# Optimization experiments

Measured on AMD Instinct MI355X. Metric: run time of the kernel, lower is better.

Reference implementation:

```python
import jax, jax.numpy as jnp
import numpy as np

B, C, L = 16, 256, 2048

def setup_inputs() -> dict:
    key = jax.random.key(0)
    k1, k2, k3, k4 = jax.random.split(key, 4)
    return {
        "proj_query": jax.random.normal(k1, (B, C, L), dtype=jnp.float32),
        "proj_key": jax.random.normal(k2, (B, C, L), dtype=jnp.float32),
        "proj_val": jax.random.normal(k3, (B, C, L), dtype=jnp.float32),
        "padding_mask": jax.random.uniform(k4, (B, 1, L), dtype=jnp.float32),
    }

def reference(proj_query, proj_key, proj_val, padding_mask):
    c = proj_query.shape[1]
    # energy[b,l,m] = sum_c Q[b,c,l] * K[b,c,m]  -> (B, L, L)
    energy = jnp.einsum("bcl,bcm->blm", proj_query, proj_key) / jnp.sqrt(jnp.float32(c))
    # log-additive padding mask (the tril mask in the source is dead code, never applied)
    logits = energy + jnp.log(padding_mask + 1e-9)
    attention = jax.nn.softmax(logits, axis=-1)
    # post-softmax multiplicative mask
    attention = attention * padding_mask
    # out[b,c,l] = sum_m V[b,c,m] * attention[b,l,m]  -> (B, C, L)
    out = jnp.einsum("bcm,blm->bcl", proj_val, attention)
    return out
```

## Files before the change

kernel.cpp:

```cpp
#include <hip/hip_runtime.h>
#include <hip/hip_bf16.h>

#define B_ 16
#define C_ 256
#define L_ 2048
#define MT 32

typedef __attribute__((ext_vector_type(8))) short bf16x8;
typedef __attribute__((ext_vector_type(4))) float f32x4;

__device__ __forceinline__ short f2bf_rne(float f) {
    union { float f; unsigned u; } x; x.f = f;
    unsigned r = x.u + 0x7fffu + ((x.u >> 16) & 1u);
    return (short)(r >> 16);
}

__device__ __forceinline__ void gld_lds16(const void* g, void* l) {
    __builtin_amdgcn_global_load_lds(
        (const __attribute__((address_space(1))) void*)g,
        (__attribute__((address_space(3))) void*)l, 16, 0, 0);
}

__global__ __launch_bounds__(256) void prepass_kernel(
        const float* __restrict__ Qin, const float* __restrict__ Kin,
        const float* __restrict__ Vin, const float* __restrict__ mask,
        short* __restrict__ Qt, short* __restrict__ Kt, short* __restrict__ Vb) {
    const int bid = blockIdx.x;
    const int t = threadIdx.x;
    if (bid < 4096) {
        __shared__ unsigned short tile[64 * 65];
        const int tens = bid >> 11;
        const int b  = (bid >> 7) & 15;
        const int c0 = ((bid >> 5) & 3) * 64;
        const int l0 = (bid & 31) * 64;
        const float* __restrict__ src = tens ? Kin : Qin;
        short* __restrict__ dst = tens ? Kt : Qt;
        #pragma unroll
        for (int i = 0; i < 4; ++i) {
            int idx = i * 256 + t;
            int ci = idx >> 4;
            int lc = (idx & 15) * 4;
            float4 v = *(const float4*)(src + ((size_t)b * C_ + (c0 + ci)) * L_ + l0 + lc);
            tile[(lc + 0) * 65 + ci] = (unsigned short)f2bf_rne(v.x);
            tile[(lc + 1) * 65 + ci] = (unsigned short)f2bf_rne(v.y);
            tile[(lc + 2) * 65 + ci] = (unsigned short)f2bf_rne(v.z);
            tile[(lc + 3) * 65 + ci] = (unsigned short)f2bf_rne(v.w);
        }
        __syncthreads();
        #pragma unroll
        for (int i = 0; i < 8; ++i) {
            int li = 8 * i + (t >> 5);
            int cp = (t & 31) * 2;
            unsigned lo = tile[li * 65 + cp];
            unsigned hi = tile[li * 65 + cp + 1];
            *(unsigned*)(dst + ((size_t)b * L_ + (l0 + li)) * C_ + c0 + cp) = lo | (hi << 16);
        }
    } else {
        size_t e = ((size_t)(bid - 4096) * 256 + t) * 8;
        int b = (int)(e >> 19);
        int m = (int)(e & (L_ - 1));
        const float4 v0 = *(const float4*)(Vin + e);
        const float4 v1 = *(const float4*)(Vin + e + 4);
        const float* mp = mask + ((size_t)b << 11) + m;
        const float4 m0 = *(const float4*)mp;
        const float4 m1 = *(const float4*)(mp + 4);
        uint4 o;
        o.x = (unsigned)(unsigned short)f2bf_rne(v0.x * m0.x)
            | ((unsigned)(unsigned short)f2bf_rne(v0.y * m0.y) << 16);
        o.y = (unsigned)(unsigned short)f2bf_rne(v0.z * m0.z)
            | ((unsigned)(unsigned short)f2bf_rne(v0.w * m0.w) << 16);
        o.z = (unsigned)(unsigned short)f2bf_rne(v1.x * m1.x)
            | ((unsigned)(unsigned short)f2bf_rne(v1.y * m1.y) << 16);
        o.w = (unsigned)(unsigned short)f2bf_rne(v1.z * m1.z)
            | ((unsigned)(unsigned short)f2bf_rne(v1.w * m1.w) << 16);
        *(uint4*)(Vb + e) = o;
    }
}

__device__ __forceinline__ void stage_tiles(const short* __restrict__ Ksrc,
                                            const short* __restrict__ Vsrc,
                                            short* Ks, short* Vs, int m0, int t) {
    #pragma unroll
    for (int rr = 0; rr < 4; ++rr) {
        int G = rr * 256 + t;
        int m = G >> 5, p = G & 31;
        int kc = p ^ m;
        gld_lds16(Ksrc + ((size_t)(m0 + m) << 8) + kc * 8, Ks + G * 8);
    }
    #pragma unroll
    for (int rr = 0; rr < 4; ++rr) {
        int G = rr * 256 + t;
        int c = G >> 2, p = G & 3;
        int kc = p ^ (c & 3);
        gld_lds16(Vsrc + (size_t)c * L_ + m0 + kc * 8, Vs + G * 8);
    }
}

__global__ __launch_bounds__(256, 2) void attn_main(
        const short* __restrict__ Qt,
        const short* __restrict__ Kt,
        const short* __restrict__ Vb,
        const float* __restrict__ mask,
        float* __restrict__ out) {
    __shared__ __align__(16) char smem[70656];
    short* KsB0 = (short*)smem;
    short* KsB1 = (short*)(smem + 16384);
    short* VsB0 = (short*)(smem + 32768);
    short* VsB1 = (short*)(smem + 49152);
    const int t = threadIdx.x;
    const int w = t >> 6, lane = t & 63, q = lane >> 4, n = lane & 15;
    short* Pw = (short*)(smem + 65536) + w * 640;

    const int b  = blockIdx.x & 15;
    const int l0 = (blockIdx.x >> 4) * 64;

    bf16x8 qf[8];
    {
        const short* qrow = Qt + ((size_t)b * L_ + (l0 + 16 * w + n)) * C_;
        #pragma unroll
        for (int ks = 0; ks < 8; ++ks)
            qf[ks] = *(const bf16x8*)(qrow + 32 * ks + 8 * q);
    }

    const f32x4 fzero = {0.f, 0.f, 0.f, 0.f};
    f32x4 Oacc[16];
    #pragma unroll
    for (int i = 0; i < 16; ++i) Oacc[i] = fzero;
    float denom[4] = {0.f, 0.f, 0.f, 0.f};

    const short* Ksrc = Kt + (size_t)b * L_ * C_;
    const short* Vsrc = Vb + (size_t)b * C_ * L_;
    const float* mrow = mask + (size_t)b * L_;

    stage_tiles(Ksrc, Vsrc, KsB0, VsB0, 0, t);
    float wva = mrow[n] + 1e-9f;
    float wvb = mrow[16 + n] + 1e-9f;

    const float CEXP = 0.09016844005556021f;

    for (int it = 0; it < L_ / MT; ++it) {
        const int cur = it & 1;
        const short* Ks = cur ? KsB1 : KsB0;
        const short* Vs = cur ? VsB1 : VsB0;

        __syncthreads();

        float nwa = 0.f, nwb = 0.f;
        if (it + 1 < L_ / MT) {
            stage_tiles(Ksrc, Vsrc, cur ? KsB0 : KsB1, cur ? VsB0 : VsB1, (it + 1) * MT, t);
            nwa = mrow[(it + 1) * MT + n] + 1e-9f;
            nwb = mrow[(it + 1) * MT + 16 + n] + 1e-9f;
        }

        f32x4 S0 = fzero, S1 = fzero;
        #pragma unroll
        for (int ks = 0; ks < 8; ++ks) {
            int kq = 4 * ks + q;
            bf16x8 b0 = *(const bf16x8*)(Ks + n * 256 + (kq ^ n) * 8);
            S0 = __builtin_amdgcn_mfma_f32_16x16x32_bf16(qf[ks], b0, S0, 0, 0, 0);
            bf16x8 b1 = *(const bf16x8*)(Ks + (16 + n) * 256 + (kq ^ (16 + n)) * 8);
            S1 = __builtin_amdgcn_mfma_f32_16x16x32_bf16(qf[ks], b1, S1, 0, 0, 0);
        }

        #pragma unroll
        for (int r = 0; r < 4; ++r) {
            int l = 4 * q + r;
            float p0 = wva * exp2f(S0[r] * CEXP);
            denom[r] += p0;
            Pw[l * 40 + (n >> 3) * 8 + (n & 7)] = f2bf_rne(p0);
            float p1 = wvb * exp2f(S1[r] * CEXP);
            denom[r] += p1;
            Pw[l * 40 + (2 + (n >> 3)) * 8 + (n & 7)] = f2bf_rne(p1);
        }

        bf16x8 af = *(const bf16x8*)(Pw + n * 40 + q * 8);
        #pragma unroll
        for (int nt2 = 0; nt2 < 16; ++nt2) {
            int c = 16 * nt2 + n;
            bf16x8 vf = *(const bf16x8*)(Vs + c * 32 + (q ^ (c & 3)) * 8);
            Oacc[nt2] = __builtin_amdgcn_mfma_f32_16x16x32_bf16(af, vf, Oacc[nt2], 0, 0, 0);
        }

        wva = nwa; wvb = nwb;
    }

    __syncthreads();

    #pragma unroll
    for (int d = 1; d < 16; d <<= 1) {
        #pragma unroll
        for (int r = 0; r < 4; ++r)
            denom[r] += __shfl_xor(denom[r], d, 64);
    }
    float rden[4];
    #pragma unroll
    for (int r = 0; r < 4; ++r) rden[r] = 1.0f / denom[r];

    float* Osh = (float*)smem;
    #pragma unroll
    for (int nt2 = 0; nt2 < 16; ++nt2) {
        int c = 16 * nt2 + n;
        #pragma unroll
        for (int r = 0; r < 4; ++r) {
            int l = 16 * w + 4 * q + r;
            Osh[c * 65 + l] = Oacc[nt2][r] * rden[r];
        }
    }
    __syncthreads();
    float* orow = out + (size_t)b * C_ * L_ + l0;
    #pragma unroll 8
    for (int i = 0; i < 64; ++i) {
        int c = 64 * w + i;
        orow[(size_t)c * L_ + lane] = Osh[c * 65 + lane];
    }
}

extern "C" void kernel_launch(void* const* d_in, const int* in_sizes, int n_in,
                              void* d_out, int out_size, void* d_ws, size_t ws_size,
                              hipStream_t stream) {
    const float* Q    = (const float*)d_in[0];
    const float* K    = (const float*)d_in[1];
    const float* V    = (const float*)d_in[2];
    const float* mask = (const float*)d_in[3];
    float* out = (float*)d_out;

    short* Qt = (short*)d_ws;
    short* Kt = Qt + (size_t)B_ * L_ * C_;
    short* Vb = Kt + (size_t)B_ * L_ * C_;

    prepass_kernel<<<8192, 256, 0, stream>>>(Q, K, V, mask, Qt, Kt, Vb);
    attn_main<<<512, 256, 0, stream>>>(Qt, Kt, Vb, mask, out);
}
```

Before: 244.2 us.

## Repartition attention waves into 2x2 query/key split with shared P tile

The main kernel now splits each 64-row block so every wave computes scores for 32 query rows against 16 keys, reusing each K fragment across two MFMAs. The PV product is split over channel quarters, with P shared block-wide through LDS. This needs an extra barrier per iteration and a cross-wave denominator reduction through shared memory. The prepass folds the softmax exponent scale into Q, transposes whole 256-channel rows with an XOR-swizzled tile and 16-byte stores, and changes the V staging swizzle.

```diff
diff --git a/kernel.cpp b/kernel.cpp
--- a/kernel.cpp
+++ b/kernel.cpp
@@ -9,6 +9,8 @@
 typedef __attribute__((ext_vector_type(8))) short bf16x8;
 typedef __attribute__((ext_vector_type(4))) float f32x4;
 
+#define CEXP 0.09016844005556021f
+
 __device__ __forceinline__ short f2bf_rne(float f) {
     union { float f; unsigned u; } x; x.f = f;
     unsigned r = x.u + 0x7fffu + ((x.u >> 16) & 1u);
@@ -19,6 +21,13 @@
     __builtin_amdgcn_global_load_lds(
         (const __attribute__((address_space(1))) void*)g,
         (__attribute__((address_space(3))) void*)l, 16, 0, 0);
+}
+
+__device__ __forceinline__ void barrier_lds_only() {
+    asm volatile("" ::: "memory");
+    __builtin_amdgcn_s_waitcnt(0xC07F);
+    __builtin_amdgcn_s_barrier();
+    asm volatile("" ::: "memory");
 }
 
 __global__ __launch_bounds__(256) void prepass_kernel(
@@ -27,36 +36,38 @@
         short* __restrict__ Qt, short* __restrict__ Kt, short* __restrict__ Vb) {
     const int bid = blockIdx.x;
     const int t = threadIdx.x;
-    if (bid < 4096) {
-        __shared__ unsigned short tile[64 * 65];
-        const int tens = bid >> 11;
-        const int b  = (bid >> 7) & 15;
-        const int c0 = ((bid >> 5) & 3) * 64;
+    if (bid < 1024) {
+        __shared__ unsigned short tile[64 * 256];
+        const int tens = bid >> 9;
+        const int b  = (bid >> 5) & 15;
         const int l0 = (bid & 31) * 64;
         const float* __restrict__ src = tens ? Kin : Qin;
         short* __restrict__ dst = tens ? Kt : Qt;
-        #pragma unroll
-        for (int i = 0; i < 4; ++i) {
-            int idx = i * 256 + t;
+        const float scale = tens ? 1.0f : CEXP;
+        #pragma unroll
+        for (int iter = 0; iter < 16; ++iter) {
+            int idx = iter * 256 + t;
             int ci = idx >> 4;
             int lc = (idx & 15) * 4;
-            float4 v = *(const float4*)(src + ((size_t)b * C_ + (c0 + ci)) * L_ + l0 + lc);
-            tile[(lc + 0) * 65 + ci] = (unsigned short)f2bf_rne(v.x);
-            tile[(lc + 1) * 65 + ci] = (unsigned short)f2bf_rne(v.y);
-            tile[(lc + 2) * 65 + ci] = (unsigned short)f2bf_rne(v.z);
-            tile[(lc + 3) * 65 + ci] = (unsigned short)f2bf_rne(v.w);
+            float4 v = *(const float4*)(src + ((size_t)(b * C_ + ci)) * L_ + l0 + lc);
+            float vv[4] = {v.x, v.y, v.z, v.w};
+            #pragma unroll
+            for (int j = 0; j < 4; ++j) {
+                int l = lc + j;
+                tile[l * 256 + (((ci >> 3) ^ (l & 31)) << 3) + (ci & 7)] =
+                    (unsigned short)f2bf_rne(vv[j] * scale);
+            }
         }
         __syncthreads();
         #pragma unroll
-        for (int i = 0; i < 8; ++i) {
-            int li = 8 * i + (t >> 5);
-            int cp = (t & 31) * 2;
-            unsigned lo = tile[li * 65 + cp];
-            unsigned hi = tile[li * 65 + cp + 1];
-            *(unsigned*)(dst + ((size_t)b * L_ + (l0 + li)) * C_ + c0 + cp) = lo | (hi << 16);
+        for (int iter = 0; iter < 8; ++iter) {
+            int li = iter * 8 + (t >> 5);
+            int ck = t & 31;
+            uint4 val = *(const uint4*)(tile + li * 256 + ((ck ^ (li & 31)) << 3));
+            *(uint4*)(dst + ((size_t)(b * L_ + l0 + li)) * C_ + ck * 8) = val;
         }
     } else {
-        size_t e = ((size_t)(bid - 4096) * 256 + t) * 8;
+        size_t e = ((size_t)(bid - 1024) * 256 + t) * 8;
         int b = (int)(e >> 19);
         int m = (int)(e & (L_ - 1));
         const float4 v0 = *(const float4*)(Vin + e);
@@ -84,14 +95,13 @@
     for (int rr = 0; rr < 4; ++rr) {
         int G = rr * 256 + t;
         int m = G >> 5, p = G & 31;
-        int kc = p ^ m;
-        gld_lds16(Ksrc + ((size_t)(m0 + m) << 8) + kc * 8, Ks + G * 8);
+        gld_lds16(Ksrc + ((size_t)(m0 + m) << 8) + (p ^ m) * 8, Ks + G * 8);
     }
     #pragma unroll
     for (int rr = 0; rr < 4; ++rr) {
         int G = rr * 256 + t;
         int c = G >> 2, p = G & 3;
-        int kc = p ^ (c & 3);
+        int kc = (p ^ (c >> 1)) & 3;
         gld_lds16(Vsrc + (size_t)c * L_ + m0 + kc * 8, Vs + G * 8);
     }
 }
@@ -102,41 +112,45 @@
         const short* __restrict__ Vb,
         const float* __restrict__ mask,
         float* __restrict__ out) {
-    __shared__ __align__(16) char smem[70656];
+    __shared__ __align__(16) char smem[71168];
     short* KsB0 = (short*)smem;
     short* KsB1 = (short*)(smem + 16384);
     short* VsB0 = (short*)(smem + 32768);
     short* VsB1 = (short*)(smem + 49152);
+    short* Pl   = (short*)(smem + 65536);
+    float* Dsh  = (float*)(smem + 70656);
+
     const int t = threadIdx.x;
     const int w = t >> 6, lane = t & 63, q = lane >> 4, n = lane & 15;
-    short* Pw = (short*)(smem + 65536) + w * 640;
+    const int g = w & 1, mt = w >> 1;
 
     const int b  = blockIdx.x & 15;
     const int l0 = (blockIdx.x >> 4) * 64;
 
-    bf16x8 qf[8];
+    bf16x8 qf[2][8];
     {
-        const short* qrow = Qt + ((size_t)b * L_ + (l0 + 16 * w + n)) * C_;
-        #pragma unroll
-        for (int ks = 0; ks < 8; ++ks)
-            qf[ks] = *(const bf16x8*)(qrow + 32 * ks + 8 * q);
+        const short* qbase = Qt + ((size_t)b * L_ + (l0 + 32 * g)) * C_;
+        #pragma unroll
+        for (int lt = 0; lt < 2; ++lt)
+            #pragma unroll
+            for (int ks = 0; ks < 8; ++ks)
+                qf[lt][ks] = *(const bf16x8*)(qbase + (size_t)(16 * lt + n) * C_ + 32 * ks + 8 * q);
     }
 
     const f32x4 fzero = {0.f, 0.f, 0.f, 0.f};
-    f32x4 Oacc[16];
-    #pragma unroll
-    for (int i = 0; i < 16; ++i) Oacc[i] = fzero;
-    float denom[4] = {0.f, 0.f, 0.f, 0.f};
-
-    const short* Ksrc = Kt + (size_t)b * L_ * C_;
-    const short* Vsrc = Vb + (size_t)b * C_ * L_;
+    f32x4 Oacc[4][4];
+    #pragma unroll
+    for (int i = 0; i < 4; ++i)
+        #pragma unroll
+        for (int j = 0; j < 4; ++j) Oacc[i][j] = fzero;
+    float dn[2][4] = {{0.f,0.f,0.f,0.f},{0.f,0.f,0.f,0.f}};
+
+    const short* Ksrc = Kt + (size_t)b * (L_ * C_);
+    const short* Vsrc = Vb + (size_t)b * (C_ * L_);
     const float* mrow = mask + (size_t)b * L_;
 
     stage_tiles(Ksrc, Vsrc, KsB0, VsB0, 0, t);
-    float wva = mrow[n] + 1e-9f;
-    float wvb = mrow[16 + n] + 1e-9f;
-
-    const float CEXP = 0.09016844005556021f;
+    float wv = mrow[16 * mt + n] + 1e-9f;
 
     for (int it = 0; it < L_ / MT; ++it) {
         const int cur = it & 1;
@@ -145,69 +159,92 @@
 
         __syncthreads();
 
-        float nwa = 0.f, nwb = 0.f;
+        float nw = 0.f;
         if (it + 1 < L_ / MT) {
             stage_tiles(Ksrc, Vsrc, cur ? KsB0 : KsB1, cur ? VsB0 : VsB1, (it + 1) * MT, t);
-            nwa = mrow[(it + 1) * MT + n] + 1e-9f;
-            nwb = mrow[(it + 1) * MT + 16 + n] + 1e-9f;
-        }
-
+            nw = mrow[(it + 1) * MT + 16 * mt + n] + 1e-9f;
+        }
+
+        const short* Krow = Ks + (16 * mt + n) * 256;
         f32x4 S0 = fzero, S1 = fzero;
         #pragma unroll
         for (int ks = 0; ks < 8; ++ks) {
-            int kq = 4 * ks + q;
-            bf16x8 b0 = *(const bf16x8*)(Ks + n * 256 + (kq ^ n) * 8);
-            S0 = __builtin_amdgcn_mfma_f32_16x16x32_bf16(qf[ks], b0, S0, 0, 0, 0);
-            bf16x8 b1 = *(const bf16x8*)(Ks + (16 + n) * 256 + (kq ^ (16 + n)) * 8);
-            S1 = __builtin_amdgcn_mfma_f32_16x16x32_bf16(qf[ks], b1, S1, 0, 0, 0);
-        }
-
+            bf16x8 bf = *(const bf16x8*)(Krow + (((4 * ks + q) ^ (16 * mt + n)) << 3));
+            S0 = __builtin_amdgcn_mfma_f32_16x16x32_bf16(qf[0][ks], bf, S0, 0, 0, 0);
+            S1 = __builtin_amdgcn_mfma_f32_16x16x32_bf16(qf[1][ks], bf, S1, 0, 0, 0);
+        }
+
+        {
+            short* Pb = Pl + (32 * g + 4 * q) * 40 + 16 * mt + n;
+            #pragma unroll
+            for (int r = 0; r < 4; ++r) {
+                float p0 = wv * exp2f(S0[r]);
+                dn[0][r] += p0;
+                Pb[r * 40] = f2bf_rne(p0);
+                float p1 = wv * exp2f(S1[r]);
+                dn[1][r] += p1;
+                Pb[(16 * 40) + r * 40] = f2bf_rne(p1);
+            }
+        }
+
+        barrier_lds_only();
+
+        bf16x8 af[4];
+        #pragma unroll
+        for (int lt = 0; lt < 4; ++lt)
+            af[lt] = *(const bf16x8*)(Pl + (16 * lt + n) * 40 + q * 8);
+        #pragma unroll
+        for (int ct = 0; ct < 4; ++ct) {
+            int c = 64 * w + 16 * ct + n;
+            bf16x8 vf = *(const bf16x8*)(Vs + c * 32 + (((q ^ (c >> 1)) & 3) << 3));
+            #pragma unroll
+            for (int lt = 0; lt < 4; ++lt)
+                Oacc[lt][ct] = __builtin_amdgcn_mfma_f32_16x16x32_bf16(af[lt], vf, Oacc[lt][ct], 0, 0, 0);
+        }
+
+        wv = nw;
+    }
+
+    __syncthreads();
+
+    #pragma unroll
+    for (int d = 1; d < 16; d <<= 1) {
+        #pragma unroll
+        for (int lt = 0; lt < 2; ++lt)
+            #pragma unroll
+            for (int r = 0; r < 4; ++r)
+                dn[lt][r] += __shfl_xor(dn[lt][r], d, 64);
+    }
+    if (n == 0) {
+        #pragma unroll
+        for (int lt = 0; lt < 2; ++lt)
+            #pragma unroll
+            for (int r = 0; r < 4; ++r)
+                Dsh[mt * 64 + 32 * g + 16 * lt + 4 * q + r] = dn[lt][r];
+    }
+    __syncthreads();
+
+    float rden[4][4];
+    #pragma unroll
+    for (int lt = 0; lt < 4; ++lt)
         #pragma unroll
         for (int r = 0; r < 4; ++r) {
-            int l = 4 * q + r;
-            float p0 = wva * exp2f(S0[r] * CEXP);
-            denom[r] += p0;
-            Pw[l * 40 + (n >> 3) * 8 + (n & 7)] = f2bf_rne(p0);
-            float p1 = wvb * exp2f(S1[r] * CEXP);
-            denom[r] += p1;
-            Pw[l * 40 + (2 + (n >> 3)) * 8 + (n & 7)] = f2bf_rne(p1);
-        }
-
-        bf16x8 af = *(const bf16x8*)(Pw + n * 40 + q * 8);
-        #pragma unroll
-        for (int nt2 = 0; nt2 < 16; ++nt2) {
-            int c = 16 * nt2 + n;
-            bf16x8 vf = *(const bf16x8*)(Vs + c * 32 + (q ^ (c & 3)) * 8);
-            Oacc[nt2] = __builtin_amdgcn_mfma_f32_16x16x32_bf16(af, vf, Oacc[nt2], 0, 0, 0);
-        }
-
-        wva = nwa; wvb = nwb;
-    }
-
+            int l = 16 * lt + 4 * q + r;
+            rden[lt][r] = 1.0f / (Dsh[l] + Dsh[64 + l]);
+        }
+
+    float* Osh = (float*)smem;
+    #pragma unroll
+    for (int lt = 0; lt < 4; ++lt)
+        #pragma unroll
+        for (int ct = 0; ct < 4; ++ct) {
+            int c = 64 * w + 16 * ct + n;
+            #pragma unroll
+            for (int r = 0; r < 4; ++r)
+                Osh[c * 65 + 16 * lt + 4 * q + r] = Oacc[lt][ct][r] * rden[lt][r];
+        }
     __syncthreads();
-
-    #pragma unroll
-    for (int d = 1; d < 16; d <<= 1) {
-        #pragma unroll
-        for (int r = 0; r < 4; ++r)
-            denom[r] += __shfl_xor(denom[r], d, 64);
-    }
-    float rden[4];
-    #pragma unroll
-    for (int r = 0; r < 4; ++r) rden[r] = 1.0f / denom[r];
-
-    float* Osh = (float*)smem;
-    #pragma unroll
-    for (int nt2 = 0; nt2 < 16; ++nt2) {
-        int c = 16 * nt2 + n;
-        #pragma unroll
-        for (int r = 0; r < 4; ++r) {
-            int l = 16 * w + 4 * q + r;
-            Osh[c * 65 + l] = Oacc[nt2][r] * rden[r];
-        }
-    }
-    __syncthreads();
-    float* orow = out + (size_t)b * C_ * L_ + l0;
+    float* orow = out + (size_t)b * (C_ * L_) + l0;
     #pragma unroll 8
     for (int i = 0; i < 64; ++i) {
         int c = 64 * w + i;
@@ -228,6 +265,6 @@
     short* Kt = Qt + (size_t)B_ * L_ * C_;
     short* Vb = Kt + (size_t)B_ * L_ * C_;
 
-    prepass_kernel<<<8192, 256, 0, stream>>>(Q, K, V, mask, Qt, Kt, Vb);
+    prepass_kernel<<<5120, 256, 0, stream>>>(Q, K, V, mask, Qt, Kt, Vb);
     attn_main<<<512, 256, 0, stream>>>(Qt, Kt, Vb, mask, out);
 }
```

Result: faster. 231.6 us (-5.2%).
